# Optimization experiments

Hardware: AMD Instinct MI355X
Metric: run time of the kernel (lower is better)

The kernel has to match this reference:

```python
import jax, jax.numpy as jnp
import numpy as np

B, N, K, H = 1, 8192, 32, 16
FIBER_IN = (16, 8)
NC_OUT = {'00': 8, '10': 8, '01': 4, '11': 4}
# (pair_key, nc_in, nc_out, num_freq) with num_freq = 2*min(di,do)+1
PAIRS = (('00', 16, 8, 1), ('10', 8, 8, 1), ('01', 16, 4, 1), ('11', 8, 4, 3))


def _silu(x):
    return x * jax.nn.sigmoid(x)


def _ln(x, g):
    mu = x.mean(-1, keepdims=True)
    var = ((x - mu) ** 2).mean(-1, keepdims=True)
    return (x - mu) * jax.lax.rsqrt(var + 1e-5) * g


def _radial(feat, p):
    # Linear -> SiLU -> LayerNorm -> Linear -> SiLU -> LayerNorm -> Linear
    w1, b1, g1, w2, b2, g2, w3, b3 = p
    h = _ln(_silu(feat @ w1 + b1), g1)
    h = _ln(_silu(h @ w2 + b2), g2)
    return h @ w3 + b3


def _lin(x, w):
    # degreewise Linear: einsum('... d m, d e -> ... e m')
    return jnp.einsum('bndm,de->bnem', x, w)


def _forward(x0, x1, rel_dist, bases, w_xi, w_xj, rps, w_out, w_si, nbr_idx, nbr_mask):
    inp = {0: x0, 1: x1}
    xi = {d: _lin(inp[d], w_xi[d]) for d in (0, 1)}
    xj = {d: _lin(inp[d], w_xj[d]) for d in (0, 1)}
    gather = jax.vmap(lambda f, i: f[i])  # per batch: [n,d,m],[n,k] -> [n,k,d,m]
    mask = nbr_mask.astype(x0.dtype)  # [b,n,k]
    denom = jnp.maximum(mask.sum(-1), 1.0)[..., None, None]  # [b,n,1,1]
    b, n, k = nbr_idx.shape
    outs = {}
    for do in (0, 1):
        chunks = []
        for di in (0, 1):
            pkey = str(di) + str(do)
            ci, co = FIBER_IN[di], NC_OUT[pkey]
            nf = 2 * min(di, do) + 1
            xg = gather(xj[di], nbr_idx) + xi[di][:, :, None]  # [b,n,k,ci,mi]
            R = _radial(rel_dist, rps[pkey]).reshape(b, n, k, co, ci, nf)
            Bt = bases[pkey].reshape(b, n, k, 2 * do + 1, 2 * di + 1, nf)  # [b,n,k,mo,mi,nf]
            # kernel = sum_f R[...,o,i,f] * B[...,mo,mi,f]; out = kernel @ x  (done in 2 cheap steps)
            tmp = jnp.einsum('bnkpqf,bnkiq->bnkpfi', Bt, xg)
            chunks.append(jnp.einsum('bnkoif,bnkpfi->bnkop', R, tmp))  # [b,n,k,co,mo]
        out = jnp.concatenate(chunks, axis=3)  # [b,n,k,dim_out,mo]
        outs[do] = (out * mask[..., None, None]).sum(2) / denom  # masked mean over neighbors
    o0 = _lin(outs[0], w_out[0]) + _lin(x0, w_si[0])
    o1 = _lin(outs[1], w_out[1]) + _lin(x1, w_si[1])
    return (o0, o1)


def setup_inputs():
    ks = iter(jax.random.split(jax.random.key(0), 80))
    nrm = lambda shp: jax.random.normal(next(ks), shp, jnp.float32)
    lin_w = lambda i, o: nrm((i, o)) / float(np.sqrt(i))
    d = {}
    d['x0'] = nrm((B, N, 16, 1))
    d['x1'] = nrm((B, N, 8, 3))
    d['rel_dist'] = jax.random.uniform(next(ks), (B, N, K, 1), jnp.float32)
    for nm, ci, co, nf in PAIRS:
        di, do = int(nm[0]), int(nm[1])
        d['basis_' + nm[0] + '_' + nm[1]] = nrm((B, N, K, 1, 2 * do + 1, 1, 2 * di + 1, nf))
    d['w_xi0'] = lin_w(16, 16); d['w_xi1'] = lin_w(8, 8)
    d['w_xj0'] = lin_w(16, 16); d['w_xj1'] = lin_w(8, 8)
    for nm, ci, co, nf in PAIRS:
        d['rp' + nm + '_w1'] = lin_w(1, H)
        d['rp' + nm + '_b1'] = jnp.zeros((H,), jnp.float32)
        d['rp' + nm + '_g1'] = jnp.ones((H,), jnp.float32)
        d['rp' + nm + '_w2'] = lin_w(H, H)
        d['rp' + nm + '_b2'] = jnp.zeros((H,), jnp.float32)
        d['rp' + nm + '_g2'] = jnp.ones((H,), jnp.float32)
        d['rp' + nm + '_w3'] = lin_w(H, nf * ci * co)
        d['rp' + nm + '_b3'] = jnp.zeros((nf * ci * co,), jnp.float32)
    d['w_out0'] = lin_w(16, 16); d['w_out1'] = lin_w(8, 8)
    d['w_si0'] = lin_w(16, 16); d['w_si1'] = lin_w(8, 8)
    d['neighbor_indices'] = jax.random.randint(next(ks), (B, N, K), 0, N, jnp.int32)
    d['neighbor_mask'] = jax.random.randint(next(ks), (B, N, K), 0, 2, jnp.int32).astype(bool)
    return d


def reference(x0, x1, rel_dist, basis_0_0, basis_1_0, basis_0_1, basis_1_1, w_xi0, w_xi1, w_xj0, w_xj1, rp00_w1, rp00_b1, rp00_g1, rp00_w2, rp00_b2, rp00_g2, rp00_w3, rp00_b3, rp10_w1, rp10_b1, rp10_g1, rp10_w2, rp10_b2, rp10_g2, rp10_w3, rp10_b3, rp01_w1, rp01_b1, rp01_g1, rp01_w2, rp01_b2, rp01_g2, rp01_w3, rp01_b3, rp11_w1, rp11_b1, rp11_g1, rp11_w2, rp11_b2, rp11_g2, rp11_w3, rp11_b3, w_out0, w_out1, w_si0, w_si1, neighbor_indices, neighbor_mask):
    bases = {'00': basis_0_0, '10': basis_1_0, '01': basis_0_1, '11': basis_1_1}
    rps = {
        '00': (rp00_w1, rp00_b1, rp00_g1, rp00_w2, rp00_b2, rp00_g2, rp00_w3, rp00_b3),
        '10': (rp10_w1, rp10_b1, rp10_g1, rp10_w2, rp10_b2, rp10_g2, rp10_w3, rp10_b3),
        '01': (rp01_w1, rp01_b1, rp01_g1, rp01_w2, rp01_b2, rp01_g2, rp01_w3, rp01_b3),
        '11': (rp11_w1, rp11_b1, rp11_g1, rp11_w2, rp11_b2, rp11_g2, rp11_w3, rp11_b3),
    }
    return _forward(x0, x1, rel_dist, bases, (w_xi0, w_xi1), (w_xj0, w_xj1), rps, (w_out0, w_out1), (w_si0, w_si1), neighbor_indices, neighbor_mask)
```

## Files before the change

### kernel.cpp

```cpp
#include <hip/hip_runtime.h>


#define NNODE 8192

#define XI0_OFF   0
#define XJ0_OFF   131072
#define XI1_OFF   262144
#define XJ1_OFF   458752
#define INT0_OFF  655360
#define INT1_OFF  786432
#define WTS2_OFF  983040
#define FLAG_OFF  990640

#define RAD00 0
#define RAD01 336
#define RAD10 672
#define RAD11 1008
#define RADN  1344
#define B3_00   1344
#define W3TT_00 1472
#define B3_01   3584
#define W3TT_01 3648
#define B3_10   4736
#define W3TT_10 4800
#define B3F_11  5888
#define W3TT_11 5984
#define BLOB_N  7584

#define YP 72

typedef __attribute__((ext_vector_type(8))) short short8v;
typedef __attribute__((ext_vector_type(4))) float float4v;

static __device__ __forceinline__ float fsilu(float x) {
    return x * (1.0f / (1.0f + __expf(-x)));
}

static __device__ __forceinline__ float dot16(const float* __restrict__ w, const float* h) {
    const float4* w4 = (const float4*)w;
    float4 a = w4[0], b = w4[1], c = w4[2], d = w4[3];
    float s0 = a.x * h[0];  s0 = fmaf(a.y, h[1], s0);  s0 = fmaf(a.z, h[2],  s0);  s0 = fmaf(a.w, h[3],  s0);
    float s1 = b.x * h[4];  s1 = fmaf(b.y, h[5], s1);  s1 = fmaf(b.z, h[6],  s1);  s1 = fmaf(b.w, h[7],  s1);
    float s2 = c.x * h[8];  s2 = fmaf(c.y, h[9], s2);  s2 = fmaf(c.z, h[10], s2);  s2 = fmaf(c.w, h[11], s2);
    float s3 = d.x * h[12]; s3 = fmaf(d.y, h[13], s3); s3 = fmaf(d.z, h[14], s3);  s3 = fmaf(d.w, h[15], s3);
    return (s0 + s1) + (s2 + s3);
}

static __device__ __forceinline__ void ln16ip(float* x, const float* __restrict__ g) {
    float mu = 0.f;
#pragma unroll
    for (int h = 0; h < 16; ++h) mu += x[h];
    mu *= 0.0625f;
    float var = 0.f;
#pragma unroll
    for (int h = 0; h < 16; ++h) { float d = x[h] - mu; var = fmaf(d, d, var); }
    var *= 0.0625f;
    const float s = rsqrtf(var + 1e-5f);
#pragma unroll
    for (int h = 0; h < 16; ++h) x[h] = (x[h] - mu) * s * g[h];
}

static __device__ __forceinline__ void radial16(float dist, const float* __restrict__ w, float* hh) {
    float t[16];
#pragma unroll
    for (int h = 0; h < 16; ++h) t[h] = fsilu(fmaf(dist, w[h], w[16 + h]));
    ln16ip(t, w + 32);
#pragma unroll
    for (int e = 0; e < 16; ++e) hh[e] = fsilu(w[48 + e] + dot16(w + 80 + e * 16, t));
    ln16ip(hh, w + 64);
}

static __device__ __forceinline__ short f2b(float x) {
    unsigned u = __float_as_uint(x);
    u += 0x7FFFu + ((u >> 16) & 1u);
    return (short)(u >> 16);
}

__global__ __launch_bounds__(256) void k_lin_in(
    const float* __restrict__ x0, const float* __restrict__ x1,
    const float* __restrict__ wxi0, const float* __restrict__ wxj0,
    const float* __restrict__ wxi1, const float* __restrict__ wxj1,
    float* __restrict__ xi0, float* __restrict__ xj0,
    float* __restrict__ xi1, float* __restrict__ xj1) {
    const int t = blockIdx.x * 256 + threadIdx.x;
    const int n = t >> 4, e = t & 15;
    const float* xr = x0 + n * 16;
    float si = 0.f, sj = 0.f;
#pragma unroll
    for (int d = 0; d < 16; ++d) {
        const float xv = xr[d];
        si = fmaf(xv, wxi0[d * 16 + e], si);
        sj = fmaf(xv, wxj0[d * 16 + e], sj);
    }
    xi0[t] = si; xj0[t] = sj;
    if (e < 8) {
        const float* x1r = x1 + n * 24;
#pragma unroll
        for (int m = 0; m < 3; ++m) {
            float a = 0.f, b = 0.f;
#pragma unroll
            for (int d = 0; d < 8; ++d) {
                const float xv = x1r[d * 3 + m];
                a = fmaf(xv, wxi1[d * 8 + e], a);
                b = fmaf(xv, wxj1[d * 8 + e], b);
            }
            xi1[n * 24 + e * 3 + m] = a;
            xj1[n * 24 + e * 3 + m] = b;
        }
    }
}

struct RPtrs { const float* a[32]; };

__global__ void k_wts2(RPtrs rp, const unsigned char* __restrict__ maskb,
                       float* __restrict__ wts, int* __restrict__ flagp) {
    const int tid = threadIdx.x;
    const int radO[4] = {RAD00, RAD01, RAD10, RAD11};
    const int rpi[4]  = {0, 2, 1, 3};
#pragma unroll
    for (int pp = 0; pp < 4; ++pp) {
        float* rd = wts + radO[pp];
        const float* w1 = rp.a[rpi[pp] * 8 + 0]; const float* b1 = rp.a[rpi[pp] * 8 + 1];
        const float* g1 = rp.a[rpi[pp] * 8 + 2]; const float* w2 = rp.a[rpi[pp] * 8 + 3];
        const float* b2 = rp.a[rpi[pp] * 8 + 4]; const float* g2 = rp.a[rpi[pp] * 8 + 5];
        if (tid < 16) {
            rd[tid] = w1[tid]; rd[16 + tid] = b1[tid]; rd[32 + tid] = g1[tid];
            rd[48 + tid] = b2[tid]; rd[64 + tid] = g2[tid];
        }
        { const int e = tid >> 4, h = tid & 15; rd[80 + tid] = w2[h * 16 + e]; }
    }
    {
        const float* w3 = rp.a[0 * 8 + 6]; const float* b3 = rp.a[0 * 8 + 7];
        for (int i = tid; i < 128; i += 256) wts[B3_00 + i] = b3[i];
        for (int i = tid; i < 16 * 128; i += 256) {
            const int h = i >> 7, c = i & 127;
            wts[W3TT_00 + h * 132 + c] = w3[i];
        }
    }
    {
        const float* w3 = rp.a[2 * 8 + 6]; const float* b3 = rp.a[2 * 8 + 7];
        for (int i = tid; i < 64; i += 256) wts[B3_01 + i] = b3[i];
        for (int i = tid; i < 16 * 64; i += 256) {
            const int h = i >> 6, c = i & 63;
            wts[W3TT_01 + h * 68 + c] = w3[i];
        }
    }
    {
        const float* w3 = rp.a[1 * 8 + 6]; const float* b3 = rp.a[1 * 8 + 7];
        for (int i = tid; i < 64; i += 256) wts[B3_10 + i] = b3[i];
        for (int i = tid; i < 16 * 64; i += 256) {
            const int h = i >> 6, c = i & 63;
            wts[W3TT_10 + h * 68 + c] = w3[i];
        }
    }
    {
        const float* w3 = rp.a[3 * 8 + 6]; const float* b3 = rp.a[3 * 8 + 7];
        for (int i = tid; i < 96; i += 256) {
            const int c8 = i / 3, f = i % 3;
            wts[B3F_11 + f * 32 + c8] = b3[i];
        }
        for (int i = tid; i < 16 * 96; i += 256) {
            const int h = i / 96, cc = i % 96, c8 = cc / 3, f = cc % 3;
            wts[W3TT_11 + h * 100 + f * 32 + c8] = w3[i];
        }
    }
    if (tid == 0) {
        int nz = 0;
        for (int i = 1; i < 64; ++i) if (i & 3) nz |= (int)maskb[i];
        *flagp = (nz != 0) ? 1 : 0;
    }
}

__global__ __launch_bounds__(256) void k_mfma(
    const float* __restrict__ rel,
    const float* __restrict__ b00, const float* __restrict__ b01,
    const float* __restrict__ b10, const float* __restrict__ b11,
    const int* __restrict__ nbr, const unsigned char* __restrict__ maskb,
    const float* __restrict__ xi0, const float* __restrict__ xj0,
    const float* __restrict__ xi1, const float* __restrict__ xj1,
    const float* __restrict__ wts2, const int* __restrict__ flagp,
    float* __restrict__ o0, float* __restrict__ o1) {
    __shared__ __align__(16) float blobr[RADN];
    __shared__ __align__(16) short ybuf[4][16][YP];
    __shared__ __align__(16) short hbuf[4][16][YP];

    {
        const float4* g4 = (const float4*)wts2;
        float4* s4 = (float4*)blobr;
        for (int i = threadIdx.x; i < RADN / 4; i += 256) s4[i] = g4[i];
    }
    __syncthreads();

    const int w  = threadIdx.x >> 6;
    const int l  = threadIdx.x & 63;
    const int n0 = blockIdx.x * 2;
    const int nl = n0 + (l >> 5);
    const int j  = nl * 32 + (l & 31);

    const int idx = nbr[j];
    const float dist = rel[j];
    const int bytelay = *flagp;
    const int mv = bytelay ? (int)maskb[j] : ((const int*)maskb)[j];
    const float mf = mv ? 1.f : 0.f;

    float cnt = mf;
#pragma unroll
    for (int off = 16; off > 0; off >>= 1) cnt += __shfl_xor(cnt, off);
    const float inv  = 1.f / fmaxf(cnt, 1.f);
    const float invN0 = __shfl(inv, 0);
    const float invN1 = __shfl(inv, 32);

    const int m16 = l & 15;
    const int g4i = l >> 4;
    const int rb  = g4i * 4;
    const int ks  = g4i * 8;
    const bool rv8 = (g4i < 2);
    const bool h0  = (m16 == 0);

    const short one_b = (short)0x3F80;
    const short8v ones = {one_b, one_b, one_b, one_b, one_b, one_b, one_b, one_b};
    const float4v zero4 = {0.f, 0.f, 0.f, 0.f};

    float hh[16];
    radial16(dist, blobr + w * 336, hh);
#pragma unroll
    for (int h = 0; h < 16; ++h) hbuf[w][h][l] = f2b(hh[h]);

    if (w == 0) {
        float xg0[16];
        {
            const float4* a = (const float4*)(xj0 + idx * 16);
            const float4* b = (const float4*)(xi0 + nl * 16);
#pragma unroll
            for (int q = 0; q < 4; ++q) {
                const float4 u = a[q], v = b[q];
                xg0[4 * q + 0] = (u.x + v.x) * mf; xg0[4 * q + 1] = (u.y + v.y) * mf;
                xg0[4 * q + 2] = (u.z + v.z) * mf; xg0[4 * q + 3] = (u.w + v.w) * mf;
            }
        }
        const float Bv = b00[j];
#pragma unroll
        for (int i = 0; i < 16; ++i) ybuf[w][i][l] = f2b(Bv * xg0[i]);

        const float* w3g = wts2 + W3TT_00;
        const float* b3g = wts2 + B3_00;
        float p[2][8];
#pragma unroll
        for (int a = 0; a < 2; ++a)
#pragma unroll
            for (int o = 0; o < 8; ++o) p[a][o] = 0.f;
#pragma unroll
        for (int h2 = 0; h2 < 2; ++h2) {
            const short8v bfr = *(const short8v*)&hbuf[w][m16][ks + h2 * 32];
            const short8v afr = *(const short8v*)&ybuf[w][m16][ks + h2 * 32];
            const float4v V = __builtin_amdgcn_mfma_f32_16x16x32_bf16(afr, bfr, zero4, 0, 0, 0);
            const float4v U = __builtin_amdgcn_mfma_f32_16x16x32_bf16(afr, ones, zero4, 0, 0, 0);
#pragma unroll
            for (int o = 0; o < 8; ++o) {
                const float4 w4 = *(const float4*)&w3g[m16 * 132 + o * 16 + rb];
                p[h2][o] += w4.x * V[0] + w4.y * V[1] + w4.z * V[2] + w4.w * V[3];
                const float4 bb = *(const float4*)&b3g[o * 16 + rb];
                const float du = bb.x * U[0] + bb.y * U[1] + bb.z * U[2] + bb.w * U[3];
                p[h2][o] = h0 ? p[h2][o] + du : p[h2][o];
            }
        }
#pragma unroll
        for (int off = 32; off > 0; off >>= 1)
#pragma unroll
            for (int a = 0; a < 2; ++a)
#pragma unroll
                for (int o = 0; o < 8; ++o) p[a][o] += __shfl_xor(p[a][o], off);
        if (l == 0) {
#pragma unroll
            for (int o = 0; o < 8; ++o) {
                o0[(n0 + 0) * 16 + o] = p[0][o] * invN0;
                o0[(n0 + 1) * 16 + o] = p[1][o] * invN1;
            }
        }
    } else if (w == 1) {
        float xg0[16];
        {
            const float4* a = (const float4*)(xj0 + idx * 16);
            const float4* b = (const float4*)(xi0 + nl * 16);
#pragma unroll
            for (int q = 0; q < 4; ++q) {
                const float4 u = a[q], v = b[q];
                xg0[4 * q + 0] = (u.x + v.x) * mf; xg0[4 * q + 1] = (u.y + v.y) * mf;
                xg0[4 * q + 2] = (u.z + v.z) * mf; xg0[4 * q + 3] = (u.w + v.w) * mf;
            }
        }
        const float* bp = b01 + j * 3;
        const float B0 = bp[0], B1 = bp[1], B2 = bp[2];
        const float* w3g = wts2 + W3TT_01;
        const float* b3g = wts2 + B3_01;
        float p[2][4][3];
#pragma unroll
        for (int a = 0; a < 2; ++a)
#pragma unroll
            for (int o = 0; o < 4; ++o)
#pragma unroll
                for (int m = 0; m < 3; ++m) p[a][o][m] = 0.f;
#pragma unroll
        for (int mo = 0; mo < 3; ++mo) {
            const float Bv = (mo == 0) ? B0 : ((mo == 1) ? B1 : B2);
#pragma unroll
            for (int i = 0; i < 16; ++i) ybuf[w][i][l] = f2b(Bv * xg0[i]);
#pragma unroll
            for (int h2 = 0; h2 < 2; ++h2) {
                const short8v bfr = *(const short8v*)&hbuf[w][m16][ks + h2 * 32];
                const short8v afr = *(const short8v*)&ybuf[w][m16][ks + h2 * 32];
                const float4v V = __builtin_amdgcn_mfma_f32_16x16x32_bf16(afr, bfr, zero4, 0, 0, 0);
                const float4v U = __builtin_amdgcn_mfma_f32_16x16x32_bf16(afr, ones, zero4, 0, 0, 0);
#pragma unroll
                for (int o = 0; o < 4; ++o) {
                    const float4 w4 = *(const float4*)&w3g[m16 * 68 + o * 16 + rb];
                    p[h2][o][mo] += w4.x * V[0] + w4.y * V[1] + w4.z * V[2] + w4.w * V[3];
                    const float4 bb = *(const float4*)&b3g[o * 16 + rb];
                    const float du = bb.x * U[0] + bb.y * U[1] + bb.z * U[2] + bb.w * U[3];
                    p[h2][o][mo] = h0 ? p[h2][o][mo] + du : p[h2][o][mo];
                }
            }
        }
#pragma unroll
        for (int off = 32; off > 0; off >>= 1)
#pragma unroll
            for (int a = 0; a < 2; ++a)
#pragma unroll
                for (int o = 0; o < 4; ++o)
#pragma unroll
                    for (int m = 0; m < 3; ++m) p[a][o][m] += __shfl_xor(p[a][o][m], off);
        if (l == 0) {
#pragma unroll
            for (int o = 0; o < 4; ++o)
#pragma unroll
                for (int m = 0; m < 3; ++m) {
                    o1[(n0 + 0) * 24 + o * 3 + m] = p[0][o][m] * invN0;
                    o1[(n0 + 1) * 24 + o * 3 + m] = p[1][o][m] * invN1;
                }
        }
    } else if (w == 2) {
        float xg1[8][3];
        {
            const float4* a = (const float4*)(xj1 + idx * 24);
            const float4* b = (const float4*)(xi1 + nl * 24);
            float tmp[24];
#pragma unroll
            for (int q = 0; q < 6; ++q) {
                const float4 u = a[q], v = b[q];
                tmp[4 * q + 0] = (u.x + v.x) * mf; tmp[4 * q + 1] = (u.y + v.y) * mf;
                tmp[4 * q + 2] = (u.z + v.z) * mf; tmp[4 * q + 3] = (u.w + v.w) * mf;
            }
#pragma unroll
            for (int i = 0; i < 8; ++i)
#pragma unroll
                for (int m = 0; m < 3; ++m) xg1[i][m] = tmp[i * 3 + m];
        }
        const float* bp = b10 + j * 3;
        const float B0 = bp[0], B1 = bp[1], B2 = bp[2];
#pragma unroll
        for (int i = 0; i < 8; ++i)
            ybuf[w][i][l] = f2b(fmaf(B2, xg1[i][2], fmaf(B1, xg1[i][1], B0 * xg1[i][0])));
        const float* w3g = wts2 + W3TT_10;
        const float* b3g = wts2 + B3_10;
        float p[2][8];
#pragma unroll
        for (int a = 0; a < 2; ++a)
#pragma unroll
            for (int o = 0; o < 8; ++o) p[a][o] = 0.f;
#pragma unroll
        for (int h2 = 0; h2 < 2; ++h2) {
            const short8v bfr = *(const short8v*)&hbuf[w][m16][ks + h2 * 32];
            const short8v afr = *(const short8v*)&ybuf[w][m16][ks + h2 * 32];
            const float4v V = __builtin_amdgcn_mfma_f32_16x16x32_bf16(afr, bfr, zero4, 0, 0, 0);
            const float4v U = __builtin_amdgcn_mfma_f32_16x16x32_bf16(afr, ones, zero4, 0, 0, 0);
#pragma unroll
            for (int o = 0; o < 8; ++o) {
                const float4 w4 = *(const float4*)&w3g[m16 * 68 + o * 8 + rb];
                const float dv = w4.x * V[0] + w4.y * V[1] + w4.z * V[2] + w4.w * V[3];
                p[h2][o] = rv8 ? p[h2][o] + dv : p[h2][o];
                const float4 bb = *(const float4*)&b3g[o * 8 + rb];
                const float du = bb.x * U[0] + bb.y * U[1] + bb.z * U[2] + bb.w * U[3];
                p[h2][o] = (rv8 && h0) ? p[h2][o] + du : p[h2][o];
            }
        }
#pragma unroll
        for (int off = 32; off > 0; off >>= 1)
#pragma unroll
            for (int a = 0; a < 2; ++a)
#pragma unroll
                for (int o = 0; o < 8; ++o) p[a][o] += __shfl_xor(p[a][o], off);
        if (l == 0) {
#pragma unroll
            for (int o = 0; o < 8; ++o) {
                o0[(n0 + 0) * 16 + 8 + o] = p[0][o] * invN0;
                o0[(n0 + 1) * 16 + 8 + o] = p[1][o] * invN1;
            }
        }
    } else {
        float xg1[8][3];
        {
            const float4* a = (const float4*)(xj1 + idx * 24);
            const float4* b = (const float4*)(xi1 + nl * 24);
            float tmp[24];
#pragma unroll
            for (int q = 0; q < 6; ++q) {
                const float4 u = a[q], v = b[q];
                tmp[4 * q + 0] = (u.x + v.x) * mf; tmp[4 * q + 1] = (u.y + v.y) * mf;
                tmp[4 * q + 2] = (u.z + v.z) * mf; tmp[4 * q + 3] = (u.w + v.w) * mf;
            }
#pragma unroll
            for (int i = 0; i < 8; ++i)
#pragma unroll
                for (int m = 0; m < 3; ++m) xg1[i][m] = tmp[i * 3 + m];
        }
        const float* bp = b11 + (size_t)j * 27;
        const float* w3g = wts2 + W3TT_11;
        const float* b3g = wts2 + B3F_11;
        float p[2][4][3];
#pragma unroll
        for (int a = 0; a < 2; ++a)
#pragma unroll
            for (int o = 0; o < 4; ++o)
#pragma unroll
                for (int m = 0; m < 3; ++m) p[a][o][m] = 0.f;
#pragma unroll
        for (int mo = 0; mo < 3; ++mo) {
#pragma unroll
            for (int f = 0; f < 3; ++f) {
                const float c0 = bp[mo * 9 + 0 + f], c1 = bp[mo * 9 + 3 + f], c2 = bp[mo * 9 + 6 + f];
#pragma unroll
                for (int i = 0; i < 8; ++i)
                    ybuf[w][i][l] = f2b(fmaf(c2, xg1[i][2], fmaf(c1, xg1[i][1], c0 * xg1[i][0])));
#pragma unroll
                for (int h2 = 0; h2 < 2; ++h2) {
                    const short8v bfr = *(const short8v*)&hbuf[w][m16][ks + h2 * 32];
                    const short8v afr = *(const short8v*)&ybuf[w][m16][ks + h2 * 32];
                    const float4v V = __builtin_amdgcn_mfma_f32_16x16x32_bf16(afr, bfr, zero4, 0, 0, 0);
                    const float4v U = __builtin_amdgcn_mfma_f32_16x16x32_bf16(afr, ones, zero4, 0, 0, 0);
#pragma unroll
                    for (int o = 0; o < 4; ++o) {
                        const float4 w4 = *(const float4*)&w3g[m16 * 100 + f * 32 + o * 8 + rb];
                        const float dv = w4.x * V[0] + w4.y * V[1] + w4.z * V[2] + w4.w * V[3];
                        p[h2][o][mo] = rv8 ? p[h2][o][mo] + dv : p[h2][o][mo];
                        const float4 bb = *(const float4*)&b3g[f * 32 + o * 8 + rb];
                        const float du = bb.x * U[0] + bb.y * U[1] + bb.z * U[2] + bb.w * U[3];
                        p[h2][o][mo] = (rv8 && h0) ? p[h2][o][mo] + du : p[h2][o][mo];
                    }
                }
            }
        }
#pragma unroll
        for (int off = 32; off > 0; off >>= 1)
#pragma unroll
            for (int a = 0; a < 2; ++a)
#pragma unroll
                for (int o = 0; o < 4; ++o)
#pragma unroll
                    for (int m = 0; m < 3; ++m) p[a][o][m] += __shfl_xor(p[a][o][m], off);
        if (l == 0) {
#pragma unroll
            for (int o = 0; o < 4; ++o)
#pragma unroll
                for (int m = 0; m < 3; ++m) {
                    o1[(n0 + 0) * 24 + (4 + o) * 3 + m] = p[0][o][m] * invN0;
                    o1[(n0 + 1) * 24 + (4 + o) * 3 + m] = p[1][o][m] * invN1;
                }
        }
    }
}

__global__ __launch_bounds__(256) void k_out(
    const float* __restrict__ x0, const float* __restrict__ x1,
    const float* __restrict__ i0, const float* __restrict__ i1,
    const float* __restrict__ wo0, const float* __restrict__ wo1,
    const float* __restrict__ ws0, const float* __restrict__ ws1,
    float* __restrict__ out) {
    const int t = blockIdx.x * 256 + threadIdx.x;
    if (t < 131072) {
        const int n = t >> 4, e = t & 15;
        float s = 0.f;
#pragma unroll
        for (int d = 0; d < 16; ++d) {
            s = fmaf(i0[n * 16 + d], wo0[d * 16 + e], s);
            s = fmaf(x0[n * 16 + d], ws0[d * 16 + e], s);
        }
        out[t] = s;
    } else if (t < 327680) {
        const int u = t - 131072;
        const int n = u / 24, r2 = u % 24, e = r2 / 3, m = r2 % 3;
        float s = 0.f;
#pragma unroll
        for (int d = 0; d < 8; ++d) {
            s = fmaf(i1[n * 24 + d * 3 + m], wo1[d * 8 + e], s);
            s = fmaf(x1[n * 24 + d * 3 + m], ws1[d * 8 + e], s);
        }
        out[t] = s;
    }
}

extern "C" void kernel_launch(void* const* d_in, const int* in_sizes, int n_in,
                              void* d_out, int out_size, void* d_ws, size_t ws_size,
                              hipStream_t stream) {
    const float* x0  = (const float*)d_in[0];
    const float* x1  = (const float*)d_in[1];
    const float* rel = (const float*)d_in[2];
    const float* b00 = (const float*)d_in[3];
    const float* b10 = (const float*)d_in[4];
    const float* b01 = (const float*)d_in[5];
    const float* b11 = (const float*)d_in[6];
    const float* wxi0 = (const float*)d_in[7];
    const float* wxi1 = (const float*)d_in[8];
    const float* wxj0 = (const float*)d_in[9];
    const float* wxj1 = (const float*)d_in[10];
    RPtrs rp;
    for (int i = 0; i < 32; ++i) rp.a[i] = (const float*)d_in[11 + i];
    const float* wo0 = (const float*)d_in[43];
    const float* wo1 = (const float*)d_in[44];
    const float* ws0 = (const float*)d_in[45];
    const float* ws1 = (const float*)d_in[46];
    const int* nbr = (const int*)d_in[47];
    const unsigned char* maskb = (const unsigned char*)d_in[48];

    float* ws = (float*)d_ws;
    float* xi0 = ws + XI0_OFF; float* xj0 = ws + XJ0_OFF;
    float* xi1 = ws + XI1_OFF; float* xj1 = ws + XJ1_OFF;
    float* i0  = ws + INT0_OFF; float* i1 = ws + INT1_OFF;
    float* wts2 = ws + WTS2_OFF;
    int* flagp = (int*)(ws + FLAG_OFF);

    hipLaunchKernelGGL(k_lin_in, dim3(512), dim3(256), 0, stream,
                       x0, x1, wxi0, wxj0, wxi1, wxj1, xi0, xj0, xi1, xj1);
    hipLaunchKernelGGL(k_wts2, dim3(1), dim3(256), 0, stream, rp, maskb, wts2, flagp);
    hipLaunchKernelGGL(k_mfma, dim3(4096), dim3(256), 0, stream,
                       rel, b00, b01, b10, b11, nbr, maskb,
                       xi0, xj0, xi1, xj1, wts2, flagp, i0, i1);
    hipLaunchKernelGGL(k_out, dim3(1280), dim3(256), 0, stream,
                       x0, x1, i0, i1, wo0, wo1, ws0, ws1, (float*)d_out);
}
```

Measured before the change: 125.3 us.

## Specialize blocks per pair type and stage full weight set in LDS

Previously each block handled 2 nodes with each of its 4 waves computing a different degree pair. Now blockIdx selects one pair type per block and the 4 waves handle 8 different nodes, so each block's waves follow the same path. Each block also stages that type's radial weights, W3 and bias into LDS, where before W3 and bias were read from global memory. The weight buffer is reorganised into per-type tiles of uniform size to support this. The risk is unequal work across block types, since the type-11 path does much more work.

```diff
diff --git a/kernel.cpp b/kernel.cpp
--- a/kernel.cpp
+++ b/kernel.cpp
@@ -10,22 +10,11 @@
 #define INT0_OFF  655360
 #define INT1_OFF  786432
 #define WTS2_OFF  983040
-#define FLAG_OFF  990640
-
-#define RAD00 0
-#define RAD01 336
-#define RAD10 672
-#define RAD11 1008
-#define RADN  1344
-#define B3_00   1344
-#define W3TT_00 1472
-#define B3_01   3584
-#define W3TT_01 3648
-#define B3_10   4736
-#define W3TT_10 4800
-#define B3F_11  5888
-#define W3TT_11 5984
-#define BLOB_N  7584
+#define FLAG_OFF  993344
+
+#define TSZ    2576
+#define B3OFF  336
+#define W3OFF  464
 
 #define YP 72
 
@@ -115,11 +104,11 @@
 __global__ void k_wts2(RPtrs rp, const unsigned char* __restrict__ maskb,
                        float* __restrict__ wts, int* __restrict__ flagp) {
     const int tid = threadIdx.x;
-    const int radO[4] = {RAD00, RAD01, RAD10, RAD11};
-    const int rpi[4]  = {0, 2, 1, 3};
+    const int rpi[4] = {0, 2, 1, 3};
 #pragma unroll
     for (int pp = 0; pp < 4; ++pp) {
-        float* rd = wts + radO[pp];
+        float* base = wts + pp * TSZ;
+        float* rd = base;
         const float* w1 = rp.a[rpi[pp] * 8 + 0]; const float* b1 = rp.a[rpi[pp] * 8 + 1];
         const float* g1 = rp.a[rpi[pp] * 8 + 2]; const float* w2 = rp.a[rpi[pp] * 8 + 3];
         const float* b2 = rp.a[rpi[pp] * 8 + 4]; const float* g2 = rp.a[rpi[pp] * 8 + 5];
@@ -130,38 +119,42 @@
         { const int e = tid >> 4, h = tid & 15; rd[80 + tid] = w2[h * 16 + e]; }
     }
     {
+        float* base = wts + 0 * TSZ;
         const float* w3 = rp.a[0 * 8 + 6]; const float* b3 = rp.a[0 * 8 + 7];
-        for (int i = tid; i < 128; i += 256) wts[B3_00 + i] = b3[i];
+        for (int i = tid; i < 128; i += 256) base[B3OFF + i] = b3[i];
         for (int i = tid; i < 16 * 128; i += 256) {
             const int h = i >> 7, c = i & 127;
-            wts[W3TT_00 + h * 132 + c] = w3[i];
+            base[W3OFF + h * 132 + c] = w3[i];
         }
     }
     {
+        float* base = wts + 1 * TSZ;
         const float* w3 = rp.a[2 * 8 + 6]; const float* b3 = rp.a[2 * 8 + 7];
-        for (int i = tid; i < 64; i += 256) wts[B3_01 + i] = b3[i];
+        for (int i = tid; i < 64; i += 256) base[B3OFF + i] = b3[i];
         for (int i = tid; i < 16 * 64; i += 256) {
             const int h = i >> 6, c = i & 63;
-            wts[W3TT_01 + h * 68 + c] = w3[i];
+            base[W3OFF + h * 68 + c] = w3[i];
         }
     }
     {
+        float* base = wts + 2 * TSZ;
         const float* w3 = rp.a[1 * 8 + 6]; const float* b3 = rp.a[1 * 8 + 7];
-        for (int i = tid; i < 64; i += 256) wts[B3_10 + i] = b3[i];
+        for (int i = tid; i < 64; i += 256) base[B3OFF + i] = b3[i];
         for (int i = tid; i < 16 * 64; i += 256) {
             const int h = i >> 6, c = i & 63;
-            wts[W3TT_10 + h * 68 + c] = w3[i];
+            base[W3OFF + h * 68 + c] = w3[i];
         }
     }
     {
+        float* base = wts + 3 * TSZ;
         const float* w3 = rp.a[3 * 8 + 6]; const float* b3 = rp.a[3 * 8 + 7];
         for (int i = tid; i < 96; i += 256) {
             const int c8 = i / 3, f = i % 3;
-            wts[B3F_11 + f * 32 + c8] = b3[i];
+            base[B3OFF + f * 32 + c8] = b3[i];
         }
         for (int i = tid; i < 16 * 96; i += 256) {
             const int h = i / 96, cc = i % 96, c8 = cc / 3, f = cc % 3;
-            wts[W3TT_11 + h * 100 + f * 32 + c8] = w3[i];
+            base[W3OFF + h * 100 + f * 32 + c8] = w3[i];
         }
     }
     if (tid == 0) {
@@ -180,20 +173,22 @@
     const float* __restrict__ xi1, const float* __restrict__ xj1,
     const float* __restrict__ wts2, const int* __restrict__ flagp,
     float* __restrict__ o0, float* __restrict__ o1) {
-    __shared__ __align__(16) float blobr[RADN];
+    __shared__ __align__(16) float blob[TSZ];
     __shared__ __align__(16) short ybuf[4][16][YP];
     __shared__ __align__(16) short hbuf[4][16][YP];
 
+    const int type = blockIdx.x & 3;
+
     {
-        const float4* g4 = (const float4*)wts2;
-        float4* s4 = (float4*)blobr;
-        for (int i = threadIdx.x; i < RADN / 4; i += 256) s4[i] = g4[i];
+        const float4* g4 = (const float4*)(wts2 + type * TSZ);
+        float4* s4 = (float4*)blob;
+        for (int i = threadIdx.x; i < TSZ / 4; i += 256) s4[i] = g4[i];
     }
     __syncthreads();
 
     const int w  = threadIdx.x >> 6;
     const int l  = threadIdx.x & 63;
-    const int n0 = blockIdx.x * 2;
+    const int n0 = (blockIdx.x >> 2) * 8 + w * 2;
     const int nl = n0 + (l >> 5);
     const int j  = nl * 32 + (l & 31);
 
@@ -222,11 +217,11 @@
     const float4v zero4 = {0.f, 0.f, 0.f, 0.f};
 
     float hh[16];
-    radial16(dist, blobr + w * 336, hh);
+    radial16(dist, blob, hh);
 #pragma unroll
     for (int h = 0; h < 16; ++h) hbuf[w][h][l] = f2b(hh[h]);
 
-    if (w == 0) {
+    if (type == 0) {
         float xg0[16];
         {
             const float4* a = (const float4*)(xj0 + idx * 16);
@@ -242,8 +237,8 @@
 #pragma unroll
         for (int i = 0; i < 16; ++i) ybuf[w][i][l] = f2b(Bv * xg0[i]);
 
-        const float* w3g = wts2 + W3TT_00;
-        const float* b3g = wts2 + B3_00;
+        const float* w3g = blob + W3OFF;
+        const float* b3g = blob + B3OFF;
         float p[2][8];
 #pragma unroll
         for (int a = 0; a < 2; ++a)
@@ -277,7 +272,7 @@
                 o0[(n0 + 1) * 16 + o] = p[1][o] * invN1;
             }
         }
-    } else if (w == 1) {
+    } else if (type == 1) {
         float xg0[16];
         {
             const float4* a = (const float4*)(xj0 + idx * 16);
@@ -291,8 +286,8 @@
         }
         const float* bp = b01 + j * 3;
         const float B0 = bp[0], B1 = bp[1], B2 = bp[2];
-        const float* w3g = wts2 + W3TT_01;
-        const float* b3g = wts2 + B3_01;
+        const float* w3g = blob + W3OFF;
+        const float* b3g = blob + B3OFF;
         float p[2][4][3];
 #pragma unroll
         for (int a = 0; a < 2; ++a)
@@ -338,7 +333,7 @@
                     o1[(n0 + 1) * 24 + o * 3 + m] = p[1][o][m] * invN1;
                 }
         }
-    } else if (w == 2) {
+    } else if (type == 2) {
         float xg1[8][3];
         {
             const float4* a = (const float4*)(xj1 + idx * 24);
@@ -360,8 +355,8 @@
 #pragma unroll
         for (int i = 0; i < 8; ++i)
             ybuf[w][i][l] = f2b(fmaf(B2, xg1[i][2], fmaf(B1, xg1[i][1], B0 * xg1[i][0])));
-        const float* w3g = wts2 + W3TT_10;
-        const float* b3g = wts2 + B3_10;
+        const float* w3g = blob + W3OFF;
+        const float* b3g = blob + B3OFF;
         float p[2][8];
 #pragma unroll
         for (int a = 0; a < 2; ++a)
@@ -414,8 +409,8 @@
                 for (int m = 0; m < 3; ++m) xg1[i][m] = tmp[i * 3 + m];
         }
         const float* bp = b11 + (size_t)j * 27;
-        const float* w3g = wts2 + W3TT_11;
-        const float* b3g = wts2 + B3F_11;
+        const float* w3g = blob + W3OFF;
+        const float* b3g = blob + B3OFF;
         float p[2][4][3];
 #pragma unroll
         for (int a = 0; a < 2; ++a)
```

New measurement: 124.0 us. About the same (-1.0%).
